# Optimization experiments

Measured on AMD Instinct MI355X. Metric: run time of the kernel, lower is better.

Reference implementation:

```python
import jax, jax.numpy as jnp
import numpy as np

BATCH, L, E = 8192, 4096, 12  # E = log2(L) butterfly stages


def setup_inputs() -> dict:
    key = jax.random.key(0)
    kx, kw = jax.random.split(key)
    x = jax.random.normal(kx, (BATCH, L), dtype=jnp.float32)
    # Stacked per-stage weights: stage s has an (L, 2) coefficient table
    # (matches nn.Parameter(torch.randn(L, 2)) for each of E stages).
    W = jax.random.normal(kw, (E, L, 2), dtype=jnp.float32)
    return {"x": x, "W": W}


def _butterfly(x, W):
    # rightmost=True: apply the smallest-stride factor first (stride 1 -> L/2).
    B = x.shape[0]
    e = W.shape[0]
    y = x
    for s in range(e):
        d = 1 << s                      # pairing stride at this stage
        g = L // (2 * d)                # number of butterfly groups
        yr = y.reshape(B, g, 2, d)      # pairs (i, i ^ d) along last dim
        Wr = W[s].reshape(g, 2, d, 2)   # per-row 2x2 mix coefficients
        top, bot = yr[:, :, 0, :], yr[:, :, 1, :]
        new_top = Wr[:, 0, :, 0] * top + Wr[:, 0, :, 1] * bot
        new_bot = Wr[:, 1, :, 0] * bot + Wr[:, 1, :, 1] * top
        y = jnp.stack([new_top, new_bot], axis=2).reshape(B, L)
    return y


def reference(x, W):
    return _butterfly(x, W)
```

## Files before the change

kernel.cpp:

```cpp
#include <hip/hip_runtime.h>


constexpr int LROW = 4096;
constexpr int RPB  = 4;
constexpr int NBLK = 8192 / RPB;

__device__ __forceinline__ int sig(int p) { return p ^ ((p >> 5) & 31); }

__global__ __launch_bounds__(256, 2)
void butterfly12_kernel(const float* __restrict__ x,
                        const float* __restrict__ W,
                        float* __restrict__ out)
{
    __shared__ float lds[RPB * LROW];

    const int t    = threadIdx.x;
    const int hi   = t >> 4;
    const int lo   = t & 15;
    const int row0 = blockIdx.x * RPB;

    float v[RPB][16];

    #pragma unroll
    for (int r = 0; r < RPB; ++r) {
        const float4* xr = reinterpret_cast<const float4*>(x + (size_t)(row0 + r) * LROW);
        #pragma unroll
        for (int m = 0; m < 4; ++m) {
            const float4 q = xr[t * 4 + m];
            v[r][4*m+0] = q.x; v[r][4*m+1] = q.y;
            v[r][4*m+2] = q.z; v[r][4*m+3] = q.w;
        }
    }

    #pragma unroll
    for (int b = 0; b < 4; ++b) {
        const int s = b;
        float2 ws[16];
        const float4* wq = reinterpret_cast<const float4*>(W + ((size_t)s * LROW + t * 16) * 2);
        #pragma unroll
        for (int m = 0; m < 8; ++m) {
            const float4 q = wq[m];
            ws[2*m]   = make_float2(q.x, q.y);
            ws[2*m+1] = make_float2(q.z, q.w);
        }
        const int dl = 1 << b;
        #pragma unroll
        for (int g = 0; g < 16; g += 2*dl)
            #pragma unroll
            for (int m = 0; m < dl; ++m) {
                const int a = g + m, c = a + dl;
                #pragma unroll
                for (int r = 0; r < RPB; ++r) {
                    const float va = v[r][a], vb = v[r][c];
                    v[r][a] = ws[a].x * va + ws[a].y * vb;
                    v[r][c] = ws[c].x * vb + ws[c].y * va;
                }
            }
    }

    #pragma unroll
    for (int r = 0; r < RPB; ++r)
        #pragma unroll
        for (int i = 0; i < 16; ++i)
            lds[r * LROW + sig(16*t + i)] = v[r][i];
    __syncthreads();
    #pragma unroll
    for (int r = 0; r < RPB; ++r)
        #pragma unroll
        for (int j = 0; j < 16; ++j)
            v[r][j] = lds[r * LROW + sig(hi*256 + j*16 + lo)];

    #pragma unroll
    for (int b = 0; b < 4; ++b) {
        const int s = 4 + b;
        float2 ws[16];
        #pragma unroll
        for (int j = 0; j < 16; ++j)
            ws[j] = *reinterpret_cast<const float2*>(W + ((size_t)s * LROW + hi*256 + j*16 + lo) * 2);
        const int dl = 1 << b;
        #pragma unroll
        for (int g = 0; g < 16; g += 2*dl)
            #pragma unroll
            for (int m = 0; m < dl; ++m) {
                const int a = g + m, c = a + dl;
                #pragma unroll
                for (int r = 0; r < RPB; ++r) {
                    const float va = v[r][a], vb = v[r][c];
                    v[r][a] = ws[a].x * va + ws[a].y * vb;
                    v[r][c] = ws[c].x * vb + ws[c].y * va;
                }
            }
    }

    #pragma unroll
    for (int r = 0; r < RPB; ++r)
        #pragma unroll
        for (int j = 0; j < 16; ++j)
            lds[r * LROW + sig(hi*256 + j*16 + lo)] = v[r][j];
    __syncthreads();
    #pragma unroll
    for (int r = 0; r < RPB; ++r)
        #pragma unroll
        for (int k = 0; k < 16; ++k)
            v[r][k] = lds[r * LROW + sig(k*256 + t)];

    #pragma unroll
    for (int b = 0; b < 4; ++b) {
        const int s = 8 + b;
        float2 ws[16];
        #pragma unroll
        for (int k = 0; k < 16; ++k)
            ws[k] = *reinterpret_cast<const float2*>(W + ((size_t)s * LROW + k*256 + t) * 2);
        const int dl = 1 << b;
        #pragma unroll
        for (int g = 0; g < 16; g += 2*dl)
            #pragma unroll
            for (int m = 0; m < dl; ++m) {
                const int a = g + m, c = a + dl;
                #pragma unroll
                for (int r = 0; r < RPB; ++r) {
                    const float va = v[r][a], vb = v[r][c];
                    v[r][a] = ws[a].x * va + ws[a].y * vb;
                    v[r][c] = ws[c].x * vb + ws[c].y * va;
                }
            }
    }

    #pragma unroll
    for (int r = 0; r < RPB; ++r) {
        float* orow = out + (size_t)(row0 + r) * LROW;
        #pragma unroll
        for (int k = 0; k < 16; ++k)
            orow[k*256 + t] = v[r][k];
    }
}

extern "C" void kernel_launch(void* const* d_in, const int* in_sizes, int n_in,
                              void* d_out, int out_size, void* d_ws, size_t ws_size,
                              hipStream_t stream) {
    const float* x = (const float*)d_in[0];
    const float* W = (const float*)d_in[1];
    float* out = (float*)d_out;

    butterfly12_kernel<<<NBLK, 256, 0, stream>>>(x, W, out);
}
```

Measured before the change: 276.8 us.

## Halve LDS footprint with float2-packed row pairs and raise occupancy target

```diff
diff --git a/kernel.cpp b/kernel.cpp
--- a/kernel.cpp
+++ b/kernel.cpp
@@ -5,25 +5,23 @@
 constexpr int RPB  = 4;
 constexpr int NBLK = 8192 / RPB;
 
-__device__ __forceinline__ int sig(int p) { return p ^ ((p >> 5) & 31); }
-
-__global__ __launch_bounds__(256, 2)
+__global__ __launch_bounds__(256, 5)
 void butterfly12_kernel(const float* __restrict__ x,
                         const float* __restrict__ W,
                         float* __restrict__ out)
 {
-    __shared__ float lds[RPB * LROW];
+    __shared__ float2 lds[LROW];
 
-    const int t    = threadIdx.x;
-    const int hi   = t >> 4;
-    const int lo   = t & 15;
-    const int row0 = blockIdx.x * RPB;
+    const int t  = threadIdx.x;
+    const int hi = t >> 4;
+    const int lo = t & 15;
+    const size_t row0 = (size_t)blockIdx.x * RPB;
 
     float v[RPB][16];
 
     #pragma unroll
     for (int r = 0; r < RPB; ++r) {
-        const float4* xr = reinterpret_cast<const float4*>(x + (size_t)(row0 + r) * LROW);
+        const float4* xr = reinterpret_cast<const float4*>(x + (row0 + r) * LROW);
         #pragma unroll
         for (int m = 0; m < 4; ++m) {
             const float4 q = xr[t * 4 + m];
@@ -59,16 +57,18 @@
     }
 
     #pragma unroll
-    for (int r = 0; r < RPB; ++r)
+    for (int h = 0; h < 2; ++h) {
+        if (h) __syncthreads();
         #pragma unroll
         for (int i = 0; i < 16; ++i)
-            lds[r * LROW + sig(16*t + i)] = v[r][i];
-    __syncthreads();
-    #pragma unroll
-    for (int r = 0; r < RPB; ++r)
+            lds[hi*256 + i*16 + (lo ^ i)] = make_float2(v[2*h][i], v[2*h+1][i]);
+        __syncthreads();
         #pragma unroll
-        for (int j = 0; j < 16; ++j)
-            v[r][j] = lds[r * LROW + sig(hi*256 + j*16 + lo)];
+        for (int j = 0; j < 16; ++j) {
+            const float2 q = lds[hi*256 + lo*16 + (j ^ lo)];
+            v[2*h][j] = q.x; v[2*h+1][j] = q.y;
+        }
+    }
 
     #pragma unroll
     for (int b = 0; b < 4; ++b) {
@@ -93,16 +93,19 @@
     }
 
     #pragma unroll
-    for (int r = 0; r < RPB; ++r)
+    for (int h = 0; h < 2; ++h) {
+        if (h) __syncthreads();
         #pragma unroll
         for (int j = 0; j < 16; ++j)
-            lds[r * LROW + sig(hi*256 + j*16 + lo)] = v[r][j];
-    __syncthreads();
-    #pragma unroll
-    for (int r = 0; r < RPB; ++r)
+            lds[hi*256 + lo*16 + (j ^ lo)] = make_float2(v[2*h][j], v[2*h+1][j]);
+        __syncthreads();
+        const int slot = lo*16 + (hi ^ lo);
         #pragma unroll
-        for (int k = 0; k < 16; ++k)
-            v[r][k] = lds[r * LROW + sig(k*256 + t)];
+        for (int k = 0; k < 16; ++k) {
+            const float2 q = lds[k*256 + slot];
+            v[2*h][k] = q.x; v[2*h+1][k] = q.y;
+        }
+    }
 
     #pragma unroll
     for (int b = 0; b < 4; ++b) {
@@ -128,7 +131,7 @@
 
     #pragma unroll
     for (int r = 0; r < RPB; ++r) {
-        float* orow = out + (size_t)(row0 + r) * LROW;
+        float* orow = out + (row0 + r) * LROW;
         #pragma unroll
         for (int k = 0; k < 16; ++k)
             orow[k*256 + t] = v[r][k];
```

Result: slower. 361.7 us (+30.7%).
